# Performance work log

Measured on AMD Instinct MI355X. Metric: run time of the kernel, lower is better.

The kernel has to match this reference:

```python
import jax, jax.numpy as jnp
import numpy as np

GAMMA = 0.99
NUM_QUANTILES = 50
STEP_TYPE_LAST = 2
HUBER_DELTA = 1.0

T, B, Q = 128, 512, NUM_QUANTILES


def setup_inputs() -> dict:
    key = jax.random.key(0)
    k1, k2, k3, k4, k5 = jax.random.split(key, 5)
    return {
        "reward": jax.random.normal(k1, (T, B), dtype=jnp.float32),
        "step_type": jax.random.randint(k2, (T, B), 0, 3, dtype=jnp.int32),
        "discount": jax.random.uniform(k3, (T, B), dtype=jnp.float32),
        "value": jax.random.normal(k4, (T, B, Q), dtype=jnp.float32),
        "target_value": jax.random.normal(k5, (T, B, Q), dtype=jnp.float32),
    }


def discounted_return(rewards, values, step_types, discounts):
    """alf value_ops.discounted_return: backward-in-time recurrence.

    rewards/step_types/discounts: [T, B]; values: [T, B, Q].
    Returns [T-1, B, Q]. rets[T-1]=values[T-1];
    rets[t] = is_last[t]*values[t] + (1-is_last[t])*(discounts[t+1]*rets[t+1] + rewards[t+1]).
    """
    is_last = (step_types == STEP_TYPE_LAST).astype(values.dtype)[..., None]  # [T,B,1]
    r = rewards[..., None]    # [T,B,1]
    d = discounts[..., None]  # [T,B,1]

    def step(carry, xs):
        is_last_t, v_t, r_tp1, d_tp1 = xs
        acc = carry * d_tp1 + r_tp1
        ret = is_last_t * v_t + (1.0 - is_last_t) * acc
        return ret, ret

    init = values[-1]
    xs = (is_last[:-1], values[:-1], r[1:], d[1:])
    _, rets = jax.lax.scan(step, init, xs, reverse=True)
    return rets  # [T-1, B, Q]


def huber(x):
    ax = jnp.abs(x)
    return jnp.where(ax <= HUBER_DELTA, 0.5 * x * x, HUBER_DELTA * (ax - 0.5 * HUBER_DELTA))


def reference(reward, step_type, discount, value, target_value):
    # td_lambda == 1.0 -> full discounted return (computed with no grad / detached)
    returns = jax.lax.stop_gradient(
        discounted_return(reward, target_value, step_type, discount * GAMMA))  # [T-1,B,Q]
    v = value[:-1]  # [T-1,B,Q]

    q = returns.shape[-1]
    tau = (jnp.arange(q, dtype=value.dtype) + 0.5) / q  # [Q] cdf midpoints

    # diff[..., i, j] = target_quantile_i - estimated_quantile_j
    diff = returns[..., :, None] - v[..., None, :]  # [T-1,B,Qt,Qe]
    weight = jnp.abs(tau - (jax.lax.stop_gradient(diff) < 0).astype(diff.dtype))
    loss = weight * huber(diff)
    # sum_over_quantiles=True: mean over target quantiles, sum over estimate quantiles
    loss = loss.mean(axis=-2).sum(axis=-1)  # [T-1,B]
    # tensor_extend_zero: append a zero row for the last time step -> [T,B]
    loss = jnp.concatenate([loss, jnp.zeros_like(loss[-1:])], axis=0)
    return loss
```

## Files before the change

kernel.cpp:

```cpp
#include <hip/hip_runtime.h>

#define GAMMA 0.99f
constexpr int T_DIM = 128;
constexpr int B_DIM = 512;
constexpr int Q_DIM = 50;
constexpr int TRET  = 127;
constexpr int SLOT  = 52;
constexpr int NPAIR = TRET * (Q_DIM/2);
constexpr int KEEP  = -1;

__global__ void __launch_bounds__(1024, 8) fused_kernel(
    const float* __restrict__ reward,
    const int*   __restrict__ step_type,
    const float* __restrict__ discount,
    const float* __restrict__ value,
    const float* __restrict__ tv,
    float*       __restrict__ out) {
  __shared__ __align__(16) float sret[TRET * SLOT];
  __shared__ __align__(16) float pacc[TRET * SLOT];
  __shared__ float sp[2][128], sqa[2][128], sqb[2][128];
  __shared__ int   snv[2][128];
  __shared__ float s_alpha[TRET], s_beta[TRET];
  __shared__ int   s_anchor[TRET];

  const int tid = threadIdx.x;
  const int b   = blockIdx.x;

  float p = 1.0f, qa = 0.0f, qb = 0.0f; int nv = KEEP;
  if (tid < TRET) {
    const bool  last = (step_type[tid * B_DIM + b] == 2);
    const float d    = GAMMA * discount[(tid + 1) * B_DIM + b];
    const float r    = reward[(tid + 1) * B_DIM + b];
    p  = last ? 0.0f : d;
    qa = last ? 1.0f : 0.0f;
    qb = last ? 0.0f : r;
    nv = last ? tid  : KEEP;
  } else if (tid == TRET) {
    out[TRET * B_DIM + b] = 0.0f;
  }
  if (tid < 128) { sp[0][tid] = p; sqa[0][tid] = qa; sqb[0][tid] = qb; snv[0][tid] = nv; }
  __syncthreads();

  int cur = 0;
#pragma unroll
  for (int off = 1; off < 128; off <<= 1) {
    if (tid < 128) {
      if (tid + off < 128) {
        const float p2  = sp [cur][tid + off];
        const float qa2 = sqa[cur][tid + off];
        const float qb2 = sqb[cur][tid + off];
        const int   nv2 = snv[cur][tid + off];
        qa = fmaf(p, qa2, qa);
        qb = fmaf(p, qb2, qb);
        p  = p * p2;
        nv = (nv == KEEP) ? nv2 : nv;
      }
      sp [cur ^ 1][tid] = p;
      sqa[cur ^ 1][tid] = qa;
      sqb[cur ^ 1][tid] = qb;
      snv[cur ^ 1][tid] = nv;
    }
    __syncthreads();
    cur ^= 1;
  }

  if (tid < TRET) {
    s_alpha[tid]  = p + qa;
    s_beta[tid]   = qb;
    s_anchor[tid] = (nv == KEEP) ? TRET : nv;
  }
  __syncthreads();

  for (int e = tid; e < NPAIR; e += 1024) {
    const int t = e / 25;
    const int i = (e - t * 25) * 2;
    const int n = s_anchor[t];
    const float  a  = s_alpha[t];
    const float  be = s_beta[t];
    const float2 tvv = *reinterpret_cast<const float2*>(
        &tv[(n * B_DIM + b) * Q_DIM + i]);
    *reinterpret_cast<float2*>(&sret[t * SLOT + i]) =
        make_float2(fmaf(a, tvv.x, be), fmaf(a, tvv.y, be));
  }
  __syncthreads();

  for (int s = tid; s < NPAIR; s += 1024) {
    const int t  = s / 25;
    const int j0 = (s - t * 25) * 2;
    const float2 vv = *reinterpret_cast<const float2*>(
        &value[(t * B_DIM + b) * Q_DIM + j0]);
    const float ta0 = ((float)j0 + 0.5f) * (1.0f / Q_DIM) - 0.5f;
    const float ta1 = ((float)j0 + 1.5f) * (1.0f / Q_DIM) - 0.5f;
    const float* rp = &sret[t * SLOT];

    float s1a = 0.0f, s2a = 0.0f, s1b = 0.0f, s2b = 0.0f;
    auto pair2 = [&](float reti) {
      { const float d = reti - vv.x;
        const float c = __builtin_amdgcn_fmed3f(d, -1.0f, 1.0f);
        const float e = fmaf(-0.5f, c, d);
        s1a = fmaf(e, c, s1a);
        s2a = fmaf(e, fabsf(c), s2a); }
      { const float d = reti - vv.y;
        const float c = __builtin_amdgcn_fmed3f(d, -1.0f, 1.0f);
        const float e = fmaf(-0.5f, c, d);
        s1b = fmaf(e, c, s1b);
        s2b = fmaf(e, fabsf(c), s2b); }
    };
#pragma unroll
    for (int i0 = 0; i0 < 48; i0 += 4) {
      const float4 rr = *reinterpret_cast<const float4*>(rp + i0);
      pair2(rr.x); pair2(rr.y); pair2(rr.z); pair2(rr.w);
    }
    {
      const float2 rr = *reinterpret_cast<const float2*>(rp + 48);
      pair2(rr.x); pair2(rr.y);
    }
    *reinterpret_cast<float2*>(&pacc[t * SLOT + j0]) =
        make_float2(fmaf(ta0, s2a, 0.5f * s1a), fmaf(ta1, s2b, 0.5f * s1b));
  }
  __syncthreads();

  const int w    = tid >> 6;
  const int lane = tid & 63;
#pragma unroll
  for (int k = 0; k < 8; ++k) {
    const int t = w * 8 + k;
    if (t < TRET) {
      float x = (lane < Q_DIM) ? pacc[t * SLOT + lane] : 0.0f;
#pragma unroll
      for (int off = 32; off > 0; off >>= 1)
        x += __shfl_xor(x, off, 64);
      if (lane == 0) out[t * B_DIM + b] = x * (1.0f / Q_DIM);
    }
  }
}

extern "C" void kernel_launch(void* const* d_in, const int* in_sizes, int n_in,
                              void* d_out, int out_size, void* d_ws, size_t ws_size,
                              hipStream_t stream) {
  const float* reward       = (const float*)d_in[0];
  const int*   step_type    = (const int*)  d_in[1];
  const float* discount     = (const float*)d_in[2];
  const float* value        = (const float*)d_in[3];
  const float* target_value = (const float*)d_in[4];
  float* out = (float*)d_out;

  fused_kernel<<<B_DIM, 1024, 0, stream>>>(reward, step_type, discount,
                                           value, target_value, out);
}
```

Measured before the change: 103.3 us.

## Prefetch value loads early, use wavefront-shuffle scan, split staging into two phases

```diff
diff --git a/kernel.cpp b/kernel.cpp
--- a/kernel.cpp
+++ b/kernel.cpp
@@ -7,6 +7,7 @@
 constexpr int TRET  = 127;
 constexpr int SLOT  = 52;
 constexpr int NPAIR = TRET * (Q_DIM/2);
+constexpr int ASLOT = 64 * (Q_DIM/2);
 constexpr int KEEP  = -1;
 
 __global__ void __launch_bounds__(1024, 8) fused_kernel(
@@ -18,81 +19,123 @@
     float*       __restrict__ out) {
   __shared__ __align__(16) float sret[TRET * SLOT];
   __shared__ __align__(16) float pacc[TRET * SLOT];
-  __shared__ float sp[2][128], sqa[2][128], sqb[2][128];
-  __shared__ int   snv[2][128];
   __shared__ float s_alpha[TRET], s_beta[TRET];
   __shared__ int   s_anchor[TRET];
 
   const int tid = threadIdx.x;
   const int b   = blockIdx.x;
 
-  float p = 1.0f, qa = 0.0f, qb = 0.0f; int nv = KEEP;
-  if (tid < TRET) {
-    const bool  last = (step_type[tid * B_DIM + b] == 2);
-    const float d    = GAMMA * discount[(tid + 1) * B_DIM + b];
-    const float r    = reward[(tid + 1) * B_DIM + b];
-    p  = last ? 0.0f : d;
-    qa = last ? 1.0f : 0.0f;
-    qb = last ? 0.0f : r;
-    nv = last ? tid  : KEEP;
-  } else if (tid == TRET) {
-    out[TRET * B_DIM + b] = 0.0f;
-  }
-  if (tid < 128) { sp[0][tid] = p; sqa[0][tid] = qa; sqb[0][tid] = qb; snv[0][tid] = nv; }
-  __syncthreads();
-
-  int cur = 0;
-#pragma unroll
-  for (int off = 1; off < 128; off <<= 1) {
-    if (tid < 128) {
-      if (tid + off < 128) {
-        const float p2  = sp [cur][tid + off];
-        const float qa2 = sqa[cur][tid + off];
-        const float qb2 = sqb[cur][tid + off];
-        const int   nv2 = snv[cur][tid + off];
-        qa = fmaf(p, qa2, qa);
-        qb = fmaf(p, qb2, qb);
-        p  = p * p2;
-        nv = (nv == KEEP) ? nv2 : nv;
+  const int  sa0 = tid,         sa1 = tid + 1024;
+  const int  sb0 = 1600 + tid,  sb1 = 2624 + tid;
+  const bool ha1 = (sa1 < ASLOT);
+  const bool hb1 = (sb1 < NPAIR);
+
+  auto vaddr = [&](int s) {
+    const int t  = s / 25;
+    const int j0 = (s - t * 25) * 2;
+    return (t * B_DIM + b) * Q_DIM + j0;
+  };
+  float2 va0, va1, vb0, vb1;
+  va0 = *reinterpret_cast<const float2*>(&value[vaddr(sa0)]);
+  vb0 = *reinterpret_cast<const float2*>(&value[vaddr(sb0)]);
+  if (ha1) va1 = *reinterpret_cast<const float2*>(&value[vaddr(sa1)]);
+  if (hb1) vb1 = *reinterpret_cast<const float2*>(&value[vaddr(sb1)]);
+  if (tid == 1023) out[TRET * B_DIM + b] = 0.0f;
+
+  if (tid < 64) {
+    const int t0 = tid, t1 = tid + 64;
+    const bool  last0 = (step_type[t0 * B_DIM + b] == 2);
+    const float d0    = GAMMA * discount[(t0 + 1) * B_DIM + b];
+    const float r0    = reward[(t0 + 1) * B_DIM + b];
+    float p0  = last0 ? 0.0f : d0;
+    float qa0 = last0 ? 1.0f : 0.0f;
+    float qb0 = last0 ? 0.0f : r0;
+    int   nv0 = last0 ? t0   : KEEP;
+    float p1 = 1.0f, qa1 = 0.0f, qb1 = 0.0f; int nv1 = KEEP;
+    if (t1 < TRET) {
+      const bool  last1 = (step_type[t1 * B_DIM + b] == 2);
+      const float d1    = GAMMA * discount[(t1 + 1) * B_DIM + b];
+      const float r1    = reward[(t1 + 1) * B_DIM + b];
+      p1  = last1 ? 0.0f : d1;
+      qa1 = last1 ? 1.0f : 0.0f;
+      qb1 = last1 ? 0.0f : r1;
+      nv1 = last1 ? t1   : KEEP;
+    }
+#pragma unroll
+    for (int off = 1; off < 64; off <<= 1) {
+      const int   src  = tid + off;
+      const float xp0  = __shfl(p0,  src, 64), xp1  = __shfl(p1,  src, 64);
+      const float xqa0 = __shfl(qa0, src, 64), xqa1 = __shfl(qa1, src, 64);
+      const float xqb0 = __shfl(qb0, src, 64), xqb1 = __shfl(qb1, src, 64);
+      const int   xnv0 = __shfl(nv0, src, 64), xnv1 = __shfl(nv1, src, 64);
+      const bool  inl  = (src < 64);
+      const float pp  = inl ? xp0  : xp1;
+      const float pqa = inl ? xqa0 : xqa1;
+      const float pqb = inl ? xqb0 : xqb1;
+      const int   pnv = inl ? xnv0 : xnv1;
+      qa0 = fmaf(p0, pqa, qa0);
+      qb0 = fmaf(p0, pqb, qb0);
+      p0  = p0 * pp;
+      nv0 = (nv0 == KEEP) ? pnv : nv0;
+      if (inl) {
+        qa1 = fmaf(p1, xqa1, qa1);
+        qb1 = fmaf(p1, xqb1, qb1);
+        p1  = p1 * xp1;
+        nv1 = (nv1 == KEEP) ? xnv1 : nv1;
       }
-      sp [cur ^ 1][tid] = p;
-      sqa[cur ^ 1][tid] = qa;
-      sqb[cur ^ 1][tid] = qb;
-      snv[cur ^ 1][tid] = nv;
-    }
-    __syncthreads();
-    cur ^= 1;
-  }
-
-  if (tid < TRET) {
-    s_alpha[tid]  = p + qa;
-    s_beta[tid]   = qb;
-    s_anchor[tid] = (nv == KEEP) ? TRET : nv;
-  }
-  __syncthreads();
-
-  for (int e = tid; e < NPAIR; e += 1024) {
+    }
+    qa0 = fmaf(p0, qa1, qa0);
+    qb0 = fmaf(p0, qb1, qb0);
+    p0  = p0 * p1;
+    nv0 = (nv0 == KEEP) ? nv1 : nv0;
+
+    s_alpha[t0]  = p0 + qa0;
+    s_beta[t0]   = qb0;
+    s_anchor[t0] = (nv0 == KEEP) ? TRET : nv0;
+    if (t1 < TRET) {
+      s_alpha[t1]  = p1 + qa1;
+      s_beta[t1]   = qb1;
+      s_anchor[t1] = (nv1 == KEEP) ? TRET : nv1;
+    }
+  }
+  __syncthreads();
+
+  int bt0, bi0, bt1 = 0, bi1 = 0;
+  float bA0, bB0, bA1 = 0.0f, bB1 = 0.0f;
+  float2 btv0, btv1;
+  {
+    bt0 = sb0 / 25; bi0 = (sb0 - bt0 * 25) * 2;
+    bA0 = s_alpha[bt0]; bB0 = s_beta[bt0];
+    btv0 = *reinterpret_cast<const float2*>(
+        &tv[(s_anchor[bt0] * B_DIM + b) * Q_DIM + bi0]);
+  }
+  if (hb1) {
+    bt1 = sb1 / 25; bi1 = (sb1 - bt1 * 25) * 2;
+    bA1 = s_alpha[bt1]; bB1 = s_beta[bt1];
+    btv1 = *reinterpret_cast<const float2*>(
+        &tv[(s_anchor[bt1] * B_DIM + b) * Q_DIM + bi1]);
+  }
+
+  auto stage = [&](int e) {
     const int t = e / 25;
     const int i = (e - t * 25) * 2;
-    const int n = s_anchor[t];
-    const float  a  = s_alpha[t];
-    const float  be = s_beta[t];
+    const float a  = s_alpha[t];
+    const float be = s_beta[t];
     const float2 tvv = *reinterpret_cast<const float2*>(
-        &tv[(n * B_DIM + b) * Q_DIM + i]);
+        &tv[(s_anchor[t] * B_DIM + b) * Q_DIM + i]);
     *reinterpret_cast<float2*>(&sret[t * SLOT + i]) =
         make_float2(fmaf(a, tvv.x, be), fmaf(a, tvv.y, be));
-  }
-  __syncthreads();
-
-  for (int s = tid; s < NPAIR; s += 1024) {
+  };
+  stage(sa0);
+  if (ha1) stage(sa1);
+  __syncthreads();
+
+  auto compute_slot = [&](int s, float2 vv) {
     const int t  = s / 25;
     const int j0 = (s - t * 25) * 2;
-    const float2 vv = *reinterpret_cast<const float2*>(
-        &value[(t * B_DIM + b) * Q_DIM + j0]);
     const float ta0 = ((float)j0 + 0.5f) * (1.0f / Q_DIM) - 0.5f;
     const float ta1 = ((float)j0 + 1.5f) * (1.0f / Q_DIM) - 0.5f;
     const float* rp = &sret[t * SLOT];
-
     float s1a = 0.0f, s2a = 0.0f, s1b = 0.0f, s2b = 0.0f;
     auto pair2 = [&](float reti) {
       { const float d = reti - vv.x;
@@ -117,7 +160,20 @@
     }
     *reinterpret_cast<float2*>(&pacc[t * SLOT + j0]) =
         make_float2(fmaf(ta0, s2a, 0.5f * s1a), fmaf(ta1, s2b, 0.5f * s1b));
-  }
+  };
+
+  compute_slot(sa0, va0);
+  if (ha1) compute_slot(sa1, va1);
+
+  *reinterpret_cast<float2*>(&sret[bt0 * SLOT + bi0]) =
+      make_float2(fmaf(bA0, btv0.x, bB0), fmaf(bA0, btv0.y, bB0));
+  if (hb1)
+    *reinterpret_cast<float2*>(&sret[bt1 * SLOT + bi1]) =
+        make_float2(fmaf(bA1, btv1.x, bB1), fmaf(bA1, btv1.y, bB1));
+  __syncthreads();
+
+  compute_slot(sb0, vb0);
+  if (hb1) compute_slot(sb1, vb1);
   __syncthreads();
 
   const int w    = tid >> 6;
```

Result: slower. 107.0 us (+3.6%).
